# Performance work log

Measured on AMD Instinct MI355X. Metric: run time of the kernel, lower is better.

Reference implementation:

```python
import jax, jax.numpy as jnp
import numpy as np

N, E = 20000, 5000
IN_FT, OUT_FT = 128, 128
DENSITY = 0.01  # fraction of nonzeros in the incidence matrix


def setup_inputs() -> dict:
    key = jax.random.key(0)
    kx, kh, kw, kb = jax.random.split(key, 4)
    X = jax.random.normal(kx, (N, IN_FT), dtype=jnp.float32)
    H = (jax.random.uniform(kh, (N, E)) < DENSITY).astype(jnp.float32)
    # xavier_normal_ with gain=0.01
    xav_std = 0.01 * np.sqrt(2.0 / (IN_FT + OUT_FT))
    weight_trans = jax.random.normal(kw, (IN_FT, OUT_FT), dtype=jnp.float32) * xav_std
    bias = jax.random.normal(kb, (OUT_FT,), dtype=jnp.float32) * 0.01
    return {"X": X, "H": H, "weight_trans": weight_trans, "bias": bias}


def reference(X, H, weight_trans, bias):
    # X: [N, in_ft], H: [N, E] incidence
    Xw = X @ weight_trans                      # [N, out_ft]
    DV = jnp.sum(H, axis=1) + 1e-12            # node degrees, [N]
    DE = jnp.sum(H, axis=0) + 1e-12            # hyperedge degrees, [E]
    # G = diag(1/DV) @ H @ diag(1/DE) @ H^T applied to Xw, computed in the
    # efficient order without materializing the NxN matrix G:
    M = H.T @ Xw                               # [E, out_ft]
    M = M / DE[:, None]                        # diag(1/DE) scaling
    out = H @ M                                # [N, out_ft]
    out = out / DV[:, None]                    # diag(1/DV) scaling
    out = out + bias
    return jax.nn.relu(out)
```

## Files before the change

### kernel.cpp

```cpp
#include <hip/hip_runtime.h>
#include <hip/hip_bf16.h>

typedef unsigned long long u64;

#define N_NODES 20000
#define N_EDGES 5000
#define FT 128
#define NT 20
#define NRG 313
#define ROW_U64 80
#define COL_STRIDE 5120
#define MAX_DEG 320
#define MAX_NDEG 128

__global__ __launch_bounds__(256) void x_to_bf16(
    const float2* __restrict__ X2, __hip_bfloat162* __restrict__ Xb2) {
  int i = blockIdx.x * 256 + threadIdx.x;
  Xb2[i] = __float22bfloat162_rn(X2[i]);
}

#define LOADB(dst, kb0) do {                                                   \
    _Pragma("unroll")                                                          \
    for (int k_ = 0; k_ < 8; ++k_) dst[k_] = make_float4(0.f, 0.f, 0.f, 0.f); \
    if (lv) {                                                                  \
      _Pragma("unroll")                                                        \
      for (int k_ = 0; k_ < 8; ++k_)                                           \
        dst[k_] = bp[(size_t)((kb0) + k_) * 1250];                             \
    }                                                                          \
  } while (0)

#define PROCB(src, kb0) do {                                                   \
    _Pragma("unroll")                                                          \
    for (int k_ = 0; k_ < 8; ++k_) {                                           \
      u64 b0_ = __ballot(src[k_].x != 0.f);                                    \
      u64 b1_ = __ballot(src[k_].y != 0.f);                                    \
      u64 b2_ = __ballot(src[k_].z != 0.f);                                    \
      u64 b3_ = __ballot(src[k_].w != 0.f);                                    \
      const bool keep_ = (lane == (kb0) + k_);                                 \
      m0 = keep_ ? b0_ : m0;  m1 = keep_ ? b1_ : m1;                           \
      m2 = keep_ ? b2_ : m2;  m3 = keep_ ? b3_ : m3;                           \
    }                                                                          \
  } while (0)

__global__ __launch_bounds__(256) void scan_bitmask(
    const float4* __restrict__ H4, u64* __restrict__ Hbt) {
  const int wid = threadIdx.x >> 6, lane = threadIdx.x & 63;
  const int gw = blockIdx.x * 4 + wid;
  const int t = gw % NT, rg = gw / NT;
  const int r0 = rg * 64;
  const int rows = min(64, N_NODES - r0);
  const int idx4 = t * 64 + lane;
  const bool lv = idx4 < 1250;
  const float4* bp = H4 + (size_t)r0 * 1250 + idx4;

  u64 m0 = 0, m1 = 0, m2 = 0, m3 = 0;
  float4 a[8], b[8];
  LOADB(a, 0);
  if (rows == 64) {
#pragma unroll
    for (int kb = 0; kb < 64; kb += 16) {
      LOADB(b, kb + 8);
      PROCB(a, kb);
      if (kb + 16 < 64) LOADB(a, kb + 16);
      PROCB(b, kb + 8);
    }
  } else {
    LOADB(b, 8);
    PROCB(a, 0);
    LOADB(a, 16);
    PROCB(b, 8);
    LOADB(b, 24);
    PROCB(a, 16);
    PROCB(b, 24);
  }
  if (lane < rows) {
    u64* hp = Hbt + (size_t)(r0 + lane) * ROW_U64 + t * 4;
    hp[0] = m0; hp[1] = m1; hp[2] = m2; hp[3] = m3;
  }
}

__global__ __launch_bounds__(256) void transpose_bm(
    const u64* __restrict__ Hbt, u64* __restrict__ HbtT) {
  const int wid = threadIdx.x >> 6, lane = threadIdx.x & 63;
  const int gw = blockIdx.x * 4 + wid;
  const int t = gw % NT, rg = gw / NT;
  const int r = rg * 64 + lane;
  u64 w0 = 0, w1 = 0, w2 = 0, w3 = 0;
  if (r < N_NODES) {
    const u64* hp = Hbt + (size_t)r * ROW_U64 + t * 4;
    w0 = hp[0]; w1 = hp[1]; w2 = hp[2]; w3 = hp[3];
  }
  u64 t0 = 0, t1 = 0, t2 = 0, t3 = 0;
  for (int l = 0; l < 64; ++l) {
    u64 c0 = __ballot((w0 >> l) & 1ull);
    u64 c1 = __ballot((w1 >> l) & 1ull);
    u64 c2 = __ballot((w2 >> l) & 1ull);
    u64 c3 = __ballot((w3 >> l) & 1ull);
    const bool keep = (lane == l);
    t0 = keep ? c0 : t0;  t1 = keep ? c1 : t1;
    t2 = keep ? c2 : t2;  t3 = keep ? c3 : t3;
  }
  u64* op = HbtT + (size_t)rg * COL_STRIDE + t * 256 + 4 * lane;
  op[0] = t0; op[1] = t1; op[2] = t2; op[3] = t3;
}

__global__ __launch_bounds__(256) void edge_gather(
    const __hip_bfloat162* __restrict__ Xb2,
    const u64* __restrict__ HbtT,
    float2* __restrict__ P2, int* __restrict__ de) {
  __shared__ int sidx[4][MAX_DEG];
  const int wid = threadIdx.x >> 6, lane = threadIdx.x & 63;
  const int e = blockIdx.x * 4 + wid;

  u64 cm[5];
#pragma unroll
  for (int q = 0; q < 5; ++q) {
    int u = q * 64 + lane;
    cm[q] = (u < NRG) ? HbtT[(size_t)u * COL_STRIDE + e] : 0ull;
  }
  int cnt = 0;
#pragma unroll
  for (int q = 0; q < 5; ++q) cnt += __popcll(cm[q]);
  int off = cnt;
  for (int d = 1; d < 64; d <<= 1) {
    int v = __shfl_up(off, d);
    if (lane >= d) off += v;
  }
  int total = __shfl(off, 63);
  off -= cnt;
#pragma unroll
  for (int q = 0; q < 5; ++q) {
    u64 w = cm[q];
    int rbase = q * 4096 + lane * 64;
    while (w) {
      int b = __ffsll(w) - 1;
      w &= w - 1;
      if (off < MAX_DEG) sidx[wid][off] = rbase + b;
      ++off;
    }
  }
  __builtin_amdgcn_s_waitcnt(0);
  int tt = min(total, MAX_DEG);

  float sx = 0.f, sy = 0.f;
  int g = 0;
  for (; g + 16 <= tt; g += 16) {
    int nn[16];
#pragma unroll
    for (int q = 0; q < 16; ++q) nn[q] = sidx[wid][g + q];
    float2 aa[16];
#pragma unroll
    for (int q = 0; q < 16; ++q) aa[q] = __bfloat1622float2(Xb2[nn[q] * 64 + lane]);
#pragma unroll
    for (int q = 0; q < 16; ++q) { sx += aa[q].x; sy += aa[q].y; }
  }
  for (; g < tt; ++g) {
    float2 a2 = __bfloat1622float2(Xb2[sidx[wid][g] * 64 + lane]);
    sx += a2.x; sy += a2.y;
  }
  P2[e * 64 + lane] = make_float2(sx, sy);
  if (lane == 0) de[e] = total;
}

__global__ __launch_bounds__(256) void gemm_M(
    const float* __restrict__ P, const float* __restrict__ W,
    const int* __restrict__ de, float* __restrict__ M) {
  int f = threadIdx.x & (FT - 1);
  int half = threadIdx.x >> 7;
  int base = blockIdx.x * 16 + half * 8;
#pragma unroll
  for (int g = 0; g < 8; g += 4) {
    int e = base + g;
    if (e >= N_EDGES) break;
    const float* p0 = P + (e + 0) * FT;
    const float* p1 = P + (e + 1) * FT;
    const float* p2 = P + (e + 2) * FT;
    const float* p3 = P + (e + 3) * FT;
    float a0 = 0.f, a1 = 0.f, a2 = 0.f, a3 = 0.f;
#pragma unroll 4
    for (int k = 0; k < FT; ++k) {
      float w = W[k * FT + f];
      a0 += p0[k] * w; a1 += p1[k] * w; a2 += p2[k] * w; a3 += p3[k] * w;
    }
    M[(e + 0) * FT + f] = a0 / ((float)de[e + 0] + 1e-12f);
    M[(e + 1) * FT + f] = a1 / ((float)de[e + 1] + 1e-12f);
    M[(e + 2) * FT + f] = a2 / ((float)de[e + 2] + 1e-12f);
    M[(e + 3) * FT + f] = a3 / ((float)de[e + 3] + 1e-12f);
  }
}

__global__ __launch_bounds__(256) void row_apply(
    const u64* __restrict__ Hbt,
    const float2* __restrict__ M2, const float2* __restrict__ bias2,
    float2* __restrict__ out2) {
  __shared__ int eidx[4][MAX_NDEG];
  const int wid = threadIdx.x >> 6, lane = threadIdx.x & 63;
  const int n = blockIdx.x * 4 + wid;
  const u64* hp = Hbt + (size_t)n * ROW_U64;
  u64 mlo = hp[lane];
  u64 mhi = (lane < ROW_U64 - 64) ? hp[64 + lane] : 0ull;
  int cnt = __popcll(mlo) + __popcll(mhi);
  int off = cnt;
  for (int d = 1; d < 64; d <<= 1) {
    int v = __shfl_up(off, d);
    if (lane >= d) off += v;
  }
  int total = __shfl(off, 63);
  off -= cnt;
  {
    int eb = (lane >> 2) * 256 + (lane & 3);
    u64 w = mlo;
    while (w) {
      int b = __ffsll(w) - 1; w &= w - 1;
      if (off < MAX_NDEG) eidx[wid][off] = eb + 4 * b;
      ++off;
    }
    int vp = 64 + lane;
    eb = (vp >> 2) * 256 + (vp & 3);
    w = mhi;
    while (w) {
      int b = __ffsll(w) - 1; w &= w - 1;
      if (off < MAX_NDEG) eidx[wid][off] = eb + 4 * b;
      ++off;
    }
  }
  __builtin_amdgcn_s_waitcnt(0);
  int tt = min(total, MAX_NDEG);

  float sx = 0.f, sy = 0.f;
  int g = 0;
  for (; g + 8 <= tt; g += 8) {
    int ee[8];
#pragma unroll
    for (int q = 0; q < 8; ++q) ee[q] = eidx[wid][g + q];
    float2 vv[8];
#pragma unroll
    for (int q = 0; q < 8; ++q) vv[q] = M2[(size_t)ee[q] * 64 + lane];
#pragma unroll
    for (int q = 0; q < 8; ++q) { sx += vv[q].x; sy += vv[q].y; }
  }
  for (; g < tt; ++g) {
    float2 v = M2[(size_t)eidx[wid][g] * 64 + lane];
    sx += v.x; sy += v.y;
  }
  float inv = 1.f / ((float)total + 1e-12f);
  float2 bb = bias2[lane];
  float2 o;
  o.x = fmaxf(fmaf(sx, inv, bb.x), 0.f);
  o.y = fmaxf(fmaf(sy, inv, bb.y), 0.f);
  out2[(size_t)n * 64 + lane] = o;
}

extern "C" void kernel_launch(void* const* d_in, const int* in_sizes, int n_in,
                              void* d_out, int out_size, void* d_ws, size_t ws_size,
                              hipStream_t stream) {
  const float* X    = (const float*)d_in[0];
  const float* H    = (const float*)d_in[1];
  const float* W    = (const float*)d_in[2];
  const float* bias = (const float*)d_in[3];
  float* out = (float*)d_out;

  int* ws = (int*)d_ws;
  u64* Hbt             = (u64*)ws;
  u64* HbtT            = (u64*)(ws + 3200000);
  __hip_bfloat162* Xb2 = (__hip_bfloat162*)(ws + 6476800);
  float* P             = (float*)(ws + 7756800);
  int* de              = ws + 8396800;
  float* M             = (float*)(ws + 8401920);

  x_to_bf16   <<<5000, 256, 0, stream>>>((const float2*)X, Xb2);
  scan_bitmask<<<1565, 256, 0, stream>>>((const float4*)H, Hbt);
  transpose_bm<<<1565, 256, 0, stream>>>(Hbt, HbtT);
  edge_gather <<<1250, 256, 0, stream>>>(Xb2, HbtT, (float2*)P, de);
  gemm_M      <<<313, 256, 0, stream>>>(P, W, de, M);
  row_apply   <<<5000, 256, 0, stream>>>(Hbt, (const float2*)M,
                                         (const float2*)bias, (float2*)out);
}
```

Measured before the change: 665.1 us.

## Scan H row-wise per wave with contiguous loads and double buffering

Replaces the tile-based bitmask scan, where each wave read a 64-row by 256-column block with strided loads, with a row-wise scan. Each wave now processes 4 consecutive full rows, reading each 5000-float row contiguously and building its 80 bitmask words with ballots. The next row's first half is prefetched while the current row's second half is processed. The aim is more sequential DRAM access for the 400MB H read. The trade-off is fewer waves in flight, more ballots per wave and less deep load overlap.

```diff
diff --git a/kernel.cpp b/kernel.cpp
--- a/kernel.cpp
+++ b/kernel.cpp
@@ -19,63 +19,67 @@
   Xb2[i] = __float22bfloat162_rn(X2[i]);
 }
 
-#define LOADB(dst, kb0) do {                                                   \
-    _Pragma("unroll")                                                          \
-    for (int k_ = 0; k_ < 8; ++k_) dst[k_] = make_float4(0.f, 0.f, 0.f, 0.f); \
-    if (lv) {                                                                  \
-      _Pragma("unroll")                                                        \
-      for (int k_ = 0; k_ < 8; ++k_)                                           \
-        dst[k_] = bp[(size_t)((kb0) + k_) * 1250];                             \
-    }                                                                          \
-  } while (0)
-
-#define PROCB(src, kb0) do {                                                   \
-    _Pragma("unroll")                                                          \
-    for (int k_ = 0; k_ < 8; ++k_) {                                           \
-      u64 b0_ = __ballot(src[k_].x != 0.f);                                    \
-      u64 b1_ = __ballot(src[k_].y != 0.f);                                    \
-      u64 b2_ = __ballot(src[k_].z != 0.f);                                    \
-      u64 b3_ = __ballot(src[k_].w != 0.f);                                    \
-      const bool keep_ = (lane == (kb0) + k_);                                 \
-      m0 = keep_ ? b0_ : m0;  m1 = keep_ ? b1_ : m1;                           \
-      m2 = keep_ ? b2_ : m2;  m3 = keep_ ? b3_ : m3;                           \
-    }                                                                          \
-  } while (0)
-
-__global__ __launch_bounds__(256) void scan_bitmask(
+__global__ __launch_bounds__(256) void scan_rows(
     const float4* __restrict__ H4, u64* __restrict__ Hbt) {
   const int wid = threadIdx.x >> 6, lane = threadIdx.x & 63;
   const int gw = blockIdx.x * 4 + wid;
-  const int t = gw % NT, rg = gw / NT;
-  const int r0 = rg * 64;
-  const int rows = min(64, N_NODES - r0);
-  const int idx4 = t * 64 + lane;
-  const bool lv = idx4 < 1250;
-  const float4* bp = H4 + (size_t)r0 * 1250 + idx4;
-
-  u64 m0 = 0, m1 = 0, m2 = 0, m3 = 0;
-  float4 a[8], b[8];
-  LOADB(a, 0);
-  if (rows == 64) {
-#pragma unroll
-    for (int kb = 0; kb < 64; kb += 16) {
-      LOADB(b, kb + 8);
-      PROCB(a, kb);
-      if (kb + 16 < 64) LOADB(a, kb + 16);
-      PROCB(b, kb + 8);
-    }
-  } else {
-    LOADB(b, 8);
-    PROCB(a, 0);
-    LOADB(a, 16);
-    PROCB(b, 8);
-    LOADB(b, 24);
-    PROCB(a, 16);
-    PROCB(b, 24);
-  }
-  if (lane < rows) {
-    u64* hp = Hbt + (size_t)(r0 + lane) * ROW_U64 + t * 4;
-    hp[0] = m0; hp[1] = m1; hp[2] = m2; hp[3] = m3;
+  const int r0 = gw * 4;
+  u64 mlo = 0, mhi = 0;
+  float4 A[10], B[10];
+
+  {
+    const float4* rp = H4 + (size_t)r0 * 1250;
+#pragma unroll
+    for (int q = 0; q < 10; ++q) A[q] = rp[q * 64 + lane];
+  }
+  for (int rr = 0; rr < 4; ++rr) {
+    const float4* rp = H4 + (size_t)(r0 + rr) * 1250;
+#pragma unroll
+    for (int q = 0; q < 9; ++q) B[q] = rp[(10 + q) * 64 + lane];
+    B[9] = make_float4(0.f, 0.f, 0.f, 0.f);
+    if (lane < 34) B[9] = rp[19 * 64 + lane];
+#pragma unroll
+    for (int q = 0; q < 10; ++q) {
+      u64 b0 = __ballot(A[q].x != 0.f);
+      u64 b1 = __ballot(A[q].y != 0.f);
+      u64 b2 = __ballot(A[q].z != 0.f);
+      u64 b3 = __ballot(A[q].w != 0.f);
+      int vp = 4 * q;
+      mlo = (lane == vp)     ? b0 : mlo;
+      mlo = (lane == vp + 1) ? b1 : mlo;
+      mlo = (lane == vp + 2) ? b2 : mlo;
+      mlo = (lane == vp + 3) ? b3 : mlo;
+    }
+    if (rr < 3) {
+      const float4* rn = H4 + (size_t)(r0 + rr + 1) * 1250;
+#pragma unroll
+      for (int q = 0; q < 10; ++q) A[q] = rn[q * 64 + lane];
+    }
+#pragma unroll
+    for (int q = 0; q < 10; ++q) {
+      u64 b0 = __ballot(B[q].x != 0.f);
+      u64 b1 = __ballot(B[q].y != 0.f);
+      u64 b2 = __ballot(B[q].z != 0.f);
+      u64 b3 = __ballot(B[q].w != 0.f);
+      const int g = 10 + q;
+      if (g < 16) {
+        const int vp = 4 * g;
+        mlo = (lane == vp)     ? b0 : mlo;
+        mlo = (lane == vp + 1) ? b1 : mlo;
+        mlo = (lane == vp + 2) ? b2 : mlo;
+        mlo = (lane == vp + 3) ? b3 : mlo;
+      } else {
+        const int vp = 4 * g - 64;
+        mhi = (lane == vp)     ? b0 : mhi;
+        mhi = (lane == vp + 1) ? b1 : mhi;
+        mhi = (lane == vp + 2) ? b2 : mhi;
+        mhi = (lane == vp + 3) ? b3 : mhi;
+      }
+    }
+    u64* hp = Hbt + (size_t)(r0 + rr) * ROW_U64;
+    hp[lane] = mlo;
+    if (lane < 16) hp[64 + lane] = mhi;
+    mlo = 0; mhi = 0;
   }
 }
 
@@ -269,7 +273,7 @@
   float* M             = (float*)(ws + 8401920);
 
   x_to_bf16   <<<5000, 256, 0, stream>>>((const float2*)X, Xb2);
-  scan_bitmask<<<1565, 256, 0, stream>>>((const float4*)H, Hbt);
+  scan_rows   <<<1250, 256, 0, stream>>>((const float4*)H, Hbt);
   transpose_bm<<<1565, 256, 0, stream>>>(Hbt, HbtT);
   edge_gather <<<1250, 256, 0, stream>>>(Xb2, HbtT, (float2*)P, de);
   gemm_M      <<<313, 256, 0, stream>>>(P, W, de, M);
```

Result: faster. 651.2 us (-2.1%).

## Fuse bitmask scan, transpose, and X bf16 conversion into one kernel

Applied to the files above, without the earlier changes.

Merges x_to_bf16, scan_bitmask and transpose_bm into a single launch. Extra blocks do the X-to-bf16 conversion, and each scan wave transposes its bitmask straight from registers instead of re-reading Hbt from global memory. H is now read with nontemporal loads in a simpler, non-double-buffered loop over rows. This saves two launches and a global round trip, at the cost of less explicit load pipelining in the scan.

```diff
diff --git a/kernel.cpp b/kernel.cpp
--- a/kernel.cpp
+++ b/kernel.cpp
@@ -2,6 +2,7 @@
 #include <hip/hip_bf16.h>
 
 typedef unsigned long long u64;
+typedef __attribute__((ext_vector_type(4))) float f32x4v;
 
 #define N_NODES 20000
 #define N_EDGES 5000
@@ -13,89 +14,58 @@
 #define MAX_DEG 320
 #define MAX_NDEG 128
 
-__global__ __launch_bounds__(256) void x_to_bf16(
+#define NTLOAD(p) __builtin_nontemporal_load((const f32x4v*)(p))
+
+__global__ __launch_bounds__(256) void scan_fused(
+    const float* __restrict__ H, u64* __restrict__ Hbt, u64* __restrict__ HbtT,
     const float2* __restrict__ X2, __hip_bfloat162* __restrict__ Xb2) {
-  int i = blockIdx.x * 256 + threadIdx.x;
-  Xb2[i] = __float22bfloat162_rn(X2[i]);
-}
-
-#define LOADB(dst, kb0) do {                                                   \
-    _Pragma("unroll")                                                          \
-    for (int k_ = 0; k_ < 8; ++k_) dst[k_] = make_float4(0.f, 0.f, 0.f, 0.f); \
-    if (lv) {                                                                  \
-      _Pragma("unroll")                                                        \
-      for (int k_ = 0; k_ < 8; ++k_)                                           \
-        dst[k_] = bp[(size_t)((kb0) + k_) * 1250];                             \
-    }                                                                          \
-  } while (0)
-
-#define PROCB(src, kb0) do {                                                   \
-    _Pragma("unroll")                                                          \
-    for (int k_ = 0; k_ < 8; ++k_) {                                           \
-      u64 b0_ = __ballot(src[k_].x != 0.f);                                    \
-      u64 b1_ = __ballot(src[k_].y != 0.f);                                    \
-      u64 b2_ = __ballot(src[k_].z != 0.f);                                    \
-      u64 b3_ = __ballot(src[k_].w != 0.f);                                    \
-      const bool keep_ = (lane == (kb0) + k_);                                 \
-      m0 = keep_ ? b0_ : m0;  m1 = keep_ ? b1_ : m1;                           \
-      m2 = keep_ ? b2_ : m2;  m3 = keep_ ? b3_ : m3;                           \
-    }                                                                          \
-  } while (0)
-
-__global__ __launch_bounds__(256) void scan_bitmask(
-    const float4* __restrict__ H4, u64* __restrict__ Hbt) {
   const int wid = threadIdx.x >> 6, lane = threadIdx.x & 63;
+
+  if (blockIdx.x >= 1565) {
+    for (int i = (blockIdx.x - 1565) * 256 + threadIdx.x; i < 1280000;
+         i += 320 * 256)
+      Xb2[i] = __float22bfloat162_rn(X2[i]);
+    return;
+  }
+
   const int gw = blockIdx.x * 4 + wid;
   const int t = gw % NT, rg = gw / NT;
   const int r0 = rg * 64;
   const int rows = min(64, N_NODES - r0);
   const int idx4 = t * 64 + lane;
   const bool lv = idx4 < 1250;
-  const float4* bp = H4 + (size_t)r0 * 1250 + idx4;
 
   u64 m0 = 0, m1 = 0, m2 = 0, m3 = 0;
-  float4 a[8], b[8];
-  LOADB(a, 0);
-  if (rows == 64) {
-#pragma unroll
-    for (int kb = 0; kb < 64; kb += 16) {
-      LOADB(b, kb + 8);
-      PROCB(a, kb);
-      if (kb + 16 < 64) LOADB(a, kb + 16);
-      PROCB(b, kb + 8);
-    }
-  } else {
-    LOADB(b, 8);
-    PROCB(a, 0);
-    LOADB(a, 16);
-    PROCB(b, 8);
-    LOADB(b, 24);
-    PROCB(a, 16);
-    PROCB(b, 24);
+  for (int kb = 0; kb < rows; kb += 8) {
+    f32x4v vv[8];
+#pragma unroll
+    for (int k = 0; k < 8; ++k) vv[k] = (f32x4v){0.f, 0.f, 0.f, 0.f};
+    if (lv) {
+      const float* bp = H + (size_t)(r0 + kb) * N_EDGES + idx4 * 4;
+#pragma unroll
+      for (int k = 0; k < 8; ++k) vv[k] = NTLOAD(bp + (size_t)k * N_EDGES);
+    }
+#pragma unroll
+    for (int k = 0; k < 8; ++k) {
+      u64 b0 = __ballot(vv[k].x != 0.f);
+      u64 b1 = __ballot(vv[k].y != 0.f);
+      u64 b2 = __ballot(vv[k].z != 0.f);
+      u64 b3 = __ballot(vv[k].w != 0.f);
+      const bool keep = (lane == kb + k);
+      m0 = keep ? b0 : m0;  m1 = keep ? b1 : m1;
+      m2 = keep ? b2 : m2;  m3 = keep ? b3 : m3;
+    }
   }
   if (lane < rows) {
     u64* hp = Hbt + (size_t)(r0 + lane) * ROW_U64 + t * 4;
     hp[0] = m0; hp[1] = m1; hp[2] = m2; hp[3] = m3;
   }
-}
-
-__global__ __launch_bounds__(256) void transpose_bm(
-    const u64* __restrict__ Hbt, u64* __restrict__ HbtT) {
-  const int wid = threadIdx.x >> 6, lane = threadIdx.x & 63;
-  const int gw = blockIdx.x * 4 + wid;
-  const int t = gw % NT, rg = gw / NT;
-  const int r = rg * 64 + lane;
-  u64 w0 = 0, w1 = 0, w2 = 0, w3 = 0;
-  if (r < N_NODES) {
-    const u64* hp = Hbt + (size_t)r * ROW_U64 + t * 4;
-    w0 = hp[0]; w1 = hp[1]; w2 = hp[2]; w3 = hp[3];
-  }
   u64 t0 = 0, t1 = 0, t2 = 0, t3 = 0;
   for (int l = 0; l < 64; ++l) {
-    u64 c0 = __ballot((w0 >> l) & 1ull);
-    u64 c1 = __ballot((w1 >> l) & 1ull);
-    u64 c2 = __ballot((w2 >> l) & 1ull);
-    u64 c3 = __ballot((w3 >> l) & 1ull);
+    u64 c0 = __ballot((m0 >> l) & 1ull);
+    u64 c1 = __ballot((m1 >> l) & 1ull);
+    u64 c2 = __ballot((m2 >> l) & 1ull);
+    u64 c3 = __ballot((m3 >> l) & 1ull);
     const bool keep = (lane == l);
     t0 = keep ? c0 : t0;  t1 = keep ? c1 : t1;
     t2 = keep ? c2 : t2;  t3 = keep ? c3 : t3;
@@ -268,11 +238,9 @@
   int* de              = ws + 8396800;
   float* M             = (float*)(ws + 8401920);
 
-  x_to_bf16   <<<5000, 256, 0, stream>>>((const float2*)X, Xb2);
-  scan_bitmask<<<1565, 256, 0, stream>>>((const float4*)H, Hbt);
-  transpose_bm<<<1565, 256, 0, stream>>>(Hbt, HbtT);
-  edge_gather <<<1250, 256, 0, stream>>>(Xb2, HbtT, (float2*)P, de);
-  gemm_M      <<<313, 256, 0, stream>>>(P, W, de, M);
-  row_apply   <<<5000, 256, 0, stream>>>(Hbt, (const float2*)M,
-                                         (const float2*)bias, (float2*)out);
-}
+  scan_fused <<<1885, 256, 0, stream>>>(H, Hbt, HbtT, (const float2*)X, Xb2);
+  edge_gather<<<1250, 256, 0, stream>>>(Xb2, HbtT, (float2*)P, de);
+  gemm_M     <<<313, 256, 0, stream>>>(P, W, de, M);
+  row_apply  <<<5000, 256, 0, stream>>>(Hbt, (const float2*)M,
+                                        (const float2*)bias, (float2*)out);
+}
```

Measured after the change: 611.9 us. 8.0% less time.
